# Kernel optimization log

Measured on AMD Instinct MI355X. Metric: run time of the kernel, lower is better.

## Reference

```python
import jax, jax.numpy as jnp
import numpy as np

N_PARTIAL = 128  # filter truncation length (init kwarg)


def setup_inputs() -> dict:
    key = jax.random.key(0)
    k1, k2 = jax.random.split(key)
    x = jax.random.normal(k1, (8, 768, 4096), dtype=jnp.float32)
    k = jax.random.normal(k2, (768, 4096), dtype=jnp.float32)
    return {"x": x, "k": k}


def reference(x, k):
    L = x.shape[-1]
    N = 2 * L
    x_dtype = x.dtype
    # FFT-based causal convolution with filter truncated to N_PARTIAL taps.
    x_f = jnp.fft.rfft(x.astype(jnp.float32), n=N, axis=-1)          # [B, H, N//2+1] complex64
    k_f = jnp.fft.rfft(k[..., :N_PARTIAL].astype(jnp.float32), n=N, axis=-1)  # [H, N//2+1]
    y_f = x_f * k_f                                                   # broadcast over batch
    y = jnp.fft.irfft(y_f, n=N, axis=-1)[..., :L].astype(x_dtype)     # truncate to causal length
    return y
```

## Files before the change

kernel.cpp:

```cpp
#include <hip/hip_runtime.h>

namespace {
constexpr int L_LEN   = 4096;
constexpr int NTAPS   = 128;
constexpr int NH      = 768;
constexpr int KSTRIDE = 4096;
constexpr int TPB     = 256;
constexpr int PADB    = 160;
constexpr int XB      = PADB + L_LEN;
constexpr int NP      = 5;

typedef __attribute__((ext_vector_type(8))) short  short8;
typedef __attribute__((ext_vector_type(4))) float  f32x4;

__device__ __forceinline__ unsigned swz(unsigned byte) {
    return byte ^ (((byte >> 7) & 1u) << 4);
}
__device__ __forceinline__ unsigned short f2bf(float f) {
    unsigned u = __builtin_bit_cast(unsigned, f);
    u += 0x7FFFu + ((u >> 16) & 1u);
    return (unsigned short)(u >> 16);
}
}

__global__ __launch_bounds__(TPB) void pconv_mfma(
    const float* __restrict__ x, const float* __restrict__ kf, float* __restrict__ y) {
    __shared__ float         skf[NTAPS];
    __shared__ unsigned char sxb[XB * 2];

    const int tid = threadIdx.x;
    const int row = blockIdx.x;
    const int h   = row % NH;

    if (tid < NTAPS / 4)
        ((float4*)skf)[tid] = ((const float4*)(kf + (size_t)h * KSTRIDE))[tid];

    if (tid < PADB / 4)
        *(unsigned long long*)(sxb + swz(8u * tid)) = 0ull;

    const float* xr = x + (size_t)row * L_LEN;
    #pragma unroll
    for (int s = 0; s < L_LEN / (TPB * 4); ++s) {
        const int q4 = tid + s * TPB;
        const float4 v = ((const float4*)xr)[q4];
        unsigned long long pk =
            (unsigned long long)f2bf(v.x)
          | ((unsigned long long)f2bf(v.y) << 16)
          | ((unsigned long long)f2bf(v.z) << 32)
          | ((unsigned long long)f2bf(v.w) << 48);
        *(unsigned long long*)(sxb + swz(2u * PADB + 8u * q4)) = pk;
    }
    __syncthreads();

    const int lane = tid & 63;
    const int i    = lane & 15;
    const int g    = lane >> 4;
    short8 afrag[NP];
    #pragma unroll
    for (int p = 0; p < NP; ++p) {
        const int tbase = 32 * p + 16 * (g >> 1) + i - 8 * (g & 1);
        short8 a;
        #pragma unroll
        for (int e = 0; e < 8; ++e) {
            const int t = tbase - e;
            const float kv = (t >= 0 && t < NTAPS) ? skf[t] : 0.0f;
            a[e] = (short)f2bf(kv);
        }
        afrag[p] = a;
    }

    const int wave = tid >> 6;
    float* yr = y + (size_t)row * L_LEN;
    #pragma unroll
    for (int tt = 0; tt < 4; ++tt) {
        const int m0 = (wave * 4 + tt) * 16;
        f32x4 acc = {0.f, 0.f, 0.f, 0.f};
        #pragma unroll
        for (int p = 0; p < NP; ++p) {
            const unsigned raw = 32u * (unsigned)(10 + m0 + i - 2 * p - (g >> 1))
                               + 16u * (unsigned)(g & 1);
            const short8 b = *(const short8*)(sxb + swz(raw));
            acc = __builtin_amdgcn_mfma_f32_16x16x32_bf16(afrag[p], b, acc, 0, 0, 0);
        }
        __builtin_nontemporal_store(acc, (f32x4*)(yr + 16 * (m0 + i) + 4 * g));
    }
}

extern "C" void kernel_launch(void* const* d_in, const int* in_sizes, int n_in,
                              void* d_out, int out_size, void* d_ws, size_t ws_size,
                              hipStream_t stream) {
    const float* x = (const float*)d_in[0];
    const float* k = (const float*)d_in[1];
    float* y = (float*)d_out;
    const int rows = in_sizes[0] / L_LEN;
    hipLaunchKernelGGL(pconv_mfma, dim3(rows), dim3(TPB), 0, stream, x, k, y);
}
```

Before: 35.28 us.

## Process two batch rows per block sharing filter fragments and prefetching second row

Each block now handles two rows with the same head, loading both rows' inputs into registers up front. It builds the filter fragments once and reuses them for both rows. The second row's loads overlap with the first row's MFMA compute and stores. This halves the block count and per-block filter setup, at the cost of more registers and a second LDS buffer, which may lower occupancy.

```diff
diff --git a/kernel.cpp b/kernel.cpp
--- a/kernel.cpp
+++ b/kernel.cpp
@@ -8,6 +8,7 @@
 constexpr int TPB     = 256;
 constexpr int PADB    = 160;
 constexpr int XB      = PADB + L_LEN;
+constexpr int XBB     = XB * 2;
 constexpr int NP      = 5;
 
 typedef __attribute__((ext_vector_type(8))) short  short8;
@@ -23,32 +24,44 @@
 }
 }
 
-__global__ __launch_bounds__(TPB) void pconv_mfma(
+__global__ __launch_bounds__(TPB) void pconv_mfma2(
     const float* __restrict__ x, const float* __restrict__ kf, float* __restrict__ y) {
     __shared__ float         skf[NTAPS];
-    __shared__ unsigned char sxb[XB * 2];
+    __shared__ unsigned char sxb[2][XBB];
 
     const int tid = threadIdx.x;
-    const int row = blockIdx.x;
-    const int h   = row % NH;
+    const int bid = blockIdx.x;
+    const int h   = bid % NH;
+    const int pr  = bid / NH;
+    const int rowA = (2 * pr)     * NH + h;
+    const int rowB = (2 * pr + 1) * NH + h;
+
+    const float* xrA = x + (size_t)rowA * L_LEN;
+    const float* xrB = x + (size_t)rowB * L_LEN;
+    float4 vA[4], vB[4];
+    #pragma unroll
+    for (int s = 0; s < 4; ++s) vA[s] = ((const float4*)xrA)[tid + s * TPB];
+    #pragma unroll
+    for (int s = 0; s < 4; ++s) vB[s] = ((const float4*)xrB)[tid + s * TPB];
 
     if (tid < NTAPS / 4)
         ((float4*)skf)[tid] = ((const float4*)(kf + (size_t)h * KSTRIDE))[tid];
 
-    if (tid < PADB / 4)
-        *(unsigned long long*)(sxb + swz(8u * tid)) = 0ull;
+    if (tid < PADB / 4) {
+        *(unsigned long long*)(sxb[0] + swz(8u * tid)) = 0ull;
+        *(unsigned long long*)(sxb[1] + swz(8u * tid)) = 0ull;
+    }
 
-    const float* xr = x + (size_t)row * L_LEN;
     #pragma unroll
-    for (int s = 0; s < L_LEN / (TPB * 4); ++s) {
+    for (int s = 0; s < 4; ++s) {
         const int q4 = tid + s * TPB;
-        const float4 v = ((const float4*)xr)[q4];
+        const float4 v = vA[s];
         unsigned long long pk =
             (unsigned long long)f2bf(v.x)
           | ((unsigned long long)f2bf(v.y) << 16)
           | ((unsigned long long)f2bf(v.z) << 32)
           | ((unsigned long long)f2bf(v.w) << 48);
-        *(unsigned long long*)(sxb + swz(2u * PADB + 8u * q4)) = pk;
+        *(unsigned long long*)(sxb[0] + swz(2u * PADB + 8u * q4)) = pk;
     }
     __syncthreads();
 
@@ -70,19 +83,52 @@
     }
 
     const int wave = tid >> 6;
-    float* yr = y + (size_t)row * L_LEN;
+
+    {
+        float* yr = y + (size_t)rowA * L_LEN;
+        #pragma unroll
+        for (int tt = 0; tt < 4; ++tt) {
+            const int m0 = (wave * 4 + tt) * 16;
+            f32x4 acc = {0.f, 0.f, 0.f, 0.f};
+            #pragma unroll
+            for (int p = 0; p < NP; ++p) {
+                const unsigned raw = 32u * (unsigned)(10 + m0 + i - 2 * p - (g >> 1))
+                                   + 16u * (unsigned)(g & 1);
+                const short8 b = *(const short8*)(sxb[0] + swz(raw));
+                acc = __builtin_amdgcn_mfma_f32_16x16x32_bf16(afrag[p], b, acc, 0, 0, 0);
+            }
+            __builtin_nontemporal_store(acc, (f32x4*)(yr + 16 * (m0 + i) + 4 * g));
+        }
+    }
+
     #pragma unroll
-    for (int tt = 0; tt < 4; ++tt) {
-        const int m0 = (wave * 4 + tt) * 16;
-        f32x4 acc = {0.f, 0.f, 0.f, 0.f};
+    for (int s = 0; s < 4; ++s) {
+        const int q4 = tid + s * TPB;
+        const float4 v = vB[s];
+        unsigned long long pk =
+            (unsigned long long)f2bf(v.x)
+          | ((unsigned long long)f2bf(v.y) << 16)
+          | ((unsigned long long)f2bf(v.z) << 32)
+          | ((unsigned long long)f2bf(v.w) << 48);
+        *(unsigned long long*)(sxb[1] + swz(2u * PADB + 8u * q4)) = pk;
+    }
+    __syncthreads();
+
+    {
+        float* yr = y + (size_t)rowB * L_LEN;
         #pragma unroll
-        for (int p = 0; p < NP; ++p) {
-            const unsigned raw = 32u * (unsigned)(10 + m0 + i - 2 * p - (g >> 1))
-                               + 16u * (unsigned)(g & 1);
-            const short8 b = *(const short8*)(sxb + swz(raw));
-            acc = __builtin_amdgcn_mfma_f32_16x16x32_bf16(afrag[p], b, acc, 0, 0, 0);
+        for (int tt = 0; tt < 4; ++tt) {
+            const int m0 = (wave * 4 + tt) * 16;
+            f32x4 acc = {0.f, 0.f, 0.f, 0.f};
+            #pragma unroll
+            for (int p = 0; p < NP; ++p) {
+                const unsigned raw = 32u * (unsigned)(10 + m0 + i - 2 * p - (g >> 1))
+                                   + 16u * (unsigned)(g & 1);
+                const short8 b = *(const short8*)(sxb[1] + swz(raw));
+                acc = __builtin_amdgcn_mfma_f32_16x16x32_bf16(afrag[p], b, acc, 0, 0, 0);
+            }
+            __builtin_nontemporal_store(acc, (f32x4*)(yr + 16 * (m0 + i) + 4 * g));
         }
-        __builtin_nontemporal_store(acc, (f32x4*)(yr + 16 * (m0 + i) + 4 * g));
     }
 }
 
@@ -93,5 +139,5 @@
     const float* k = (const float*)d_in[1];
     float* y = (float*)d_out;
     const int rows = in_sizes[0] / L_LEN;
-    hipLaunchKernelGGL(pconv_mfma, dim3(rows), dim3(TPB), 0, stream, x, k, y);
+    hipLaunchKernelGGL(pconv_mfma2, dim3(rows / 2), dim3(TPB), 0, stream, x, k, y);
 }
```

After: 35.38 us. No clear change (+0.3%).
